# Performance work log

Measured on AMD Instinct MI355X. Metric: run time of the kernel, lower is better.

The kernel has to match this reference:

```python
import jax, jax.numpy as jnp
import numpy as np

B, C_IN, C_OUT, H, W = 32, 64, 64, 128, 128
K, KH, KW = 4, 3, 3
HID = max(8, C_IN // 4)  # reduction=4 -> 16


def setup_inputs() -> dict:
    key = jax.random.key(0)
    ks = jax.random.split(key, 16)
    s = lambda k, shape, scale=0.1: jax.random.normal(k, shape, dtype=jnp.float32) * scale
    inp = {
        "x": jax.random.normal(ks[0], (B, C_IN, H, W), dtype=jnp.float32),
        "weight": s(ks[1], (K, C_OUT, C_IN, KH, KW)),  # static weight bank
        "bias": s(ks[2], (C_OUT,)),
        "mlp_w": s(ks[3], (HID, C_IN)),
        "mlp_b": s(ks[4], (HID,)),
        "wK": s(ks[5], (K, HID)),  "bK": s(ks[6], (K,)),
        "wO": s(ks[7], (C_OUT, HID)), "bO": s(ks[8], (C_OUT,)),
        "wI": s(ks[9], (C_IN, HID)),  "bI": s(ks[10], (C_IN,)),
        "wH": s(ks[11], (KH, HID)),   "bH": s(ks[12], (KH,)),
        "wW": s(ks[13], (KW, HID)),   "bW": s(ks[14], (KW,)),
    }
    return inp


def reference(x, weight, bias, mlp_w, mlp_b, wK, bK, wO, bO, wI, bI, wH, bH, wW, bW):
    # ---- attention branch: global avg pool -> MLP -> 5 heads ----
    g = jnp.mean(x, axis=(2, 3))                         # [B, C_in]
    h = jax.nn.relu(g @ mlp_w.T + mlp_b)                 # [B, HID]
    aK = jax.nn.softmax(h @ wK.T + bK, axis=1)           # [B, K]
    aO = jax.nn.sigmoid(h @ wO.T + bO)                   # [B, O]
    aI = jax.nn.sigmoid(h @ wI.T + bI)                   # [B, I]
    aH = jax.nn.sigmoid(h @ wH.T + bH)                   # [B, kh]
    aW = jax.nn.sigmoid(h @ wW.T + bW)                   # [B, kw]
    aH = aH / (jnp.sum(aH, axis=1, keepdims=True) + 1e-6)
    aW = aW / (jnp.sum(aW, axis=1, keepdims=True) + 1e-6)
    # fused 5-way outer product + reduction over K (same math as alpha einsum)
    w_dyn = jnp.einsum('bk,bo,bi,bh,bw,koihw->boihw', aK, aO, aI, aH, aW, weight)
    # ---- per-sample conv2d (groups=B trick expressed as vmap) ----
    def conv_one(xb, wb):
        return jax.lax.conv_general_dilated(
            xb[None], wb, window_strides=(1, 1), padding=((1, 1), (1, 1)),
            dimension_numbers=('NCHW', 'OIHW', 'NCHW'))[0]
    out = jax.vmap(conv_one)(x, w_dyn) + bias[None, :, None, None]
    return out
```

## Files before the change

### kernel.cpp

```cpp
#include <hip/hip_runtime.h>
#include <hip/hip_bf16.h>
#include <math.h>

#define BB 32
#define CI 64
#define CO 64
#define HH 128
#define WW 128
#define KK 4
#define HID 16

typedef __attribute__((ext_vector_type(8)))  __bf16 bf16x8;
typedef __attribute__((ext_vector_type(16))) float  floatx16;

__device__ __forceinline__ unsigned short f2bf(float f) {
    union { float f; unsigned int u; } a; a.f = f;
    unsigned int u = a.u;
    unsigned int r = (u + 0x7fffu + ((u >> 16) & 1u)) >> 16;
    return (unsigned short)r;
}

__global__ __launch_bounds__(256) void pool_kernel(const float* __restrict__ x,
                                                   float* __restrict__ g) {
    int bc = blockIdx.x;
    const float4* p = reinterpret_cast<const float4*>(x + (size_t)bc * (HH * WW));
    float s = 0.f;
    for (int i = threadIdx.x; i < (HH * WW) / 4; i += 256) {
        float4 v = p[i];
        s += v.x + v.y + v.z + v.w;
    }
    for (int off = 32; off > 0; off >>= 1) s += __shfl_down(s, off, 64);
    __shared__ float red[4];
    if ((threadIdx.x & 63) == 0) red[threadIdx.x >> 6] = s;
    __syncthreads();
    if (threadIdx.x == 0) {
        float tot = red[0] + red[1] + red[2] + red[3];
        g[bc] = tot * (1.0f / (HH * WW));
    }
}

__global__ __launch_bounds__(64) void attn_kernel(
    const float* __restrict__ g,
    const float* __restrict__ mlp_w, const float* __restrict__ mlp_b,
    const float* __restrict__ wK, const float* __restrict__ bK,
    const float* __restrict__ wO, const float* __restrict__ bO,
    const float* __restrict__ wI, const float* __restrict__ bI,
    const float* __restrict__ wH, const float* __restrict__ bH,
    const float* __restrict__ wW, const float* __restrict__ bW,
    float* __restrict__ aK, float* __restrict__ aO, float* __restrict__ aI,
    float* __restrict__ aH, float* __restrict__ aW) {
    int b = blockIdx.x;
    int t = threadIdx.x;
    __shared__ float sg[CI];
    __shared__ float sh[HID];
    __shared__ float sK[KK];
    __shared__ float sH[3];
    __shared__ float sW[3];

    sg[t] = g[b * CI + t];
    __syncthreads();

    if (t < HID) {
        float s = mlp_b[t];
        for (int c = 0; c < CI; c++) s = fmaf(mlp_w[t * CI + c], sg[c], s);
        sh[t] = fmaxf(s, 0.f);
    }
    __syncthreads();

    {
        float sO = bO[t], sI = bI[t];
        for (int j = 0; j < HID; j++) {
            float hv = sh[j];
            sO = fmaf(wO[t * HID + j], hv, sO);
            sI = fmaf(wI[t * HID + j], hv, sI);
        }
        aO[b * CO + t] = 1.f / (1.f + expf(-sO));
        aI[b * CI + t] = 1.f / (1.f + expf(-sI));
    }
    if (t < KK) {
        float s = bK[t];
        for (int j = 0; j < HID; j++) s = fmaf(wK[t * HID + j], sh[j], s);
        sK[t] = s;
    }
    if (t < 3) {
        float s = bH[t];
        for (int j = 0; j < HID; j++) s = fmaf(wH[t * HID + j], sh[j], s);
        sH[t] = 1.f / (1.f + expf(-s));
        float s2 = bW[t];
        for (int j = 0; j < HID; j++) s2 = fmaf(wW[t * HID + j], sh[j], s2);
        sW[t] = 1.f / (1.f + expf(-s2));
    }
    __syncthreads();

    if (t == 0) {
        float m = fmaxf(fmaxf(sK[0], sK[1]), fmaxf(sK[2], sK[3]));
        float e0 = expf(sK[0] - m), e1 = expf(sK[1] - m);
        float e2 = expf(sK[2] - m), e3 = expf(sK[3] - m);
        float s = e0 + e1 + e2 + e3;
        aK[b * KK + 0] = e0 / s;
        aK[b * KK + 1] = e1 / s;
        aK[b * KK + 2] = e2 / s;
        aK[b * KK + 3] = e3 / s;
        float hs = sH[0] + sH[1] + sH[2] + 1e-6f;
        float wsum = sW[0] + sW[1] + sW[2] + 1e-6f;
        for (int i = 0; i < 3; i++) {
            aH[b * 3 + i] = sH[i] / hs;
            aW[b * 3 + i] = sW[i] / wsum;
        }
    }
}

#define WD_TOT (BB * 9 * CO * CI)
__global__ __launch_bounds__(256) void wdyn_kernel(
    const float* __restrict__ weight,
    const float* __restrict__ aK, const float* __restrict__ aO,
    const float* __restrict__ aI, const float* __restrict__ aH,
    const float* __restrict__ aW, unsigned short* __restrict__ wdbf) {
    int idx = blockIdx.x * 256 + threadIdx.x;
    if (idx >= WD_TOT) return;
    int i   = idx & 63;
    int o   = (idx >> 6) & 63;
    int bt  = idx >> 12;
    int tap = bt % 9;
    int b   = bt / 9;

    int wbase = (o * CI + i) * 9 + tap;
    const float* ak = aK + b * KK;
    float s = 0.f;
#pragma unroll
    for (int k = 0; k < KK; k++) s = fmaf(ak[k], weight[k * (CO * CI * 9) + wbase], s);
    float v = s * aO[b * CO + o] * aI[b * CI + i] *
              aH[b * 3 + tap / 3] * aW[b * 3 + tap % 3];
    wdbf[idx] = f2bf(v);
}

#define ICCH 16
#define PADI 24
#define SX_ELE (6 * 130 * PADI)
#define SW_ELE (9 * 64 * PADI)

__global__ __launch_bounds__(512, 4) void conv_kernel(
    const float* __restrict__ x, const unsigned short* __restrict__ wdbf,
    const float* __restrict__ bias, float* __restrict__ out) {
    const int y0 = blockIdx.x * 4;
    const int b  = blockIdx.y;
    const int t  = threadIdx.x;
    const int lane = t & 63;
    const int w    = t >> 6;
    const int ry   = w >> 1;
    const int c0   = (w & 1) * 64;
    const int l31  = lane & 31;
    const int koct = lane >> 5;

    __shared__ __align__(16) unsigned short sx[SX_ELE];
    __shared__ __align__(16) unsigned short sw[SW_ELE];

    floatx16 acc[2][2];
#pragma unroll
    for (int i = 0; i < 2; i++)
#pragma unroll
        for (int j = 0; j < 2; j++)
#pragma unroll
            for (int q = 0; q < 16; q++) acc[i][j][q] = 0.f;

    const float* xb = x + (size_t)b * CI * HH * WW;
    const unsigned short* wdb = wdbf + (size_t)b * 9 * CO * CI;

    const int pA0 = (0 * 32 + l31) * PADI + koct * 8;
    const int pA1 = (1 * 32 + l31) * PADI + koct * 8;
    const int pB0 = (ry * 130 + c0 + 0  + l31) * PADI + koct * 8;
    const int pB1 = (ry * 130 + c0 + 32 + l31) * PADI + koct * 8;

    for (int chunk = 0; chunk < 4; chunk++) {
        const int ic0 = chunk * ICCH;
        __syncthreads();
        for (int idx = t; idx < 6 * 130 * 8; idx += 512) {
            int c  = idx % 130;
            int t2 = idx / 130;
            int r  = t2 % 6;
            int icp = t2 / 6;
            int gy = y0 - 1 + r;
            int gx = c - 1;
            float f0 = 0.f, f1 = 0.f;
            if ((unsigned)gy < (unsigned)HH && (unsigned)gx < (unsigned)WW) {
                const float* xp = xb + (size_t)(ic0 + icp * 2) * (HH * WW) + gy * WW + gx;
                f0 = xp[0];
                f1 = xp[HH * WW];
            }
            unsigned int pk = (unsigned int)f2bf(f0) | ((unsigned int)f2bf(f1) << 16);
            *reinterpret_cast<unsigned int*>(&sx[(r * 130 + c) * PADI + icp * 2]) = pk;
        }
        for (int idx = t; idx < 9 * 64 * 2; idx += 512) {
            int k8  = idx & 1;
            int oc  = (idx >> 1) & 63;
            int tap = idx >> 7;
            const uint4 v = *reinterpret_cast<const uint4*>(
                wdb + ((tap * 64 + oc) * 64 + ic0 + k8 * 8));
            *reinterpret_cast<uint4*>(&sw[(tap * 64 + oc) * PADI + k8 * 8]) = v;
        }
        __syncthreads();

#pragma unroll
        for (int kh = 0; kh < 3; kh++) {
#pragma unroll
            for (int kw = 0; kw < 3; kw++) {
                const int tap  = kh * 3 + kw;
                const int aoff = tap * (64 * PADI);
                const int boff = (kh * 130 + kw) * PADI;
                bf16x8 a0 = *reinterpret_cast<const bf16x8*>(&sw[pA0 + aoff]);
                bf16x8 a1 = *reinterpret_cast<const bf16x8*>(&sw[pA1 + aoff]);
                bf16x8 b0 = *reinterpret_cast<const bf16x8*>(&sx[pB0 + boff]);
                bf16x8 b1 = *reinterpret_cast<const bf16x8*>(&sx[pB1 + boff]);
                acc[0][0] = __builtin_amdgcn_mfma_f32_32x32x16_bf16(a0, b0, acc[0][0], 0, 0, 0);
                acc[0][1] = __builtin_amdgcn_mfma_f32_32x32x16_bf16(a0, b1, acc[0][1], 0, 0, 0);
                acc[1][0] = __builtin_amdgcn_mfma_f32_32x32x16_bf16(a1, b0, acc[1][0], 0, 0, 0);
                acc[1][1] = __builtin_amdgcn_mfma_f32_32x32x16_bf16(a1, b1, acc[1][1], 0, 0, 0);
            }
        }
    }

    const int y = y0 + ry;
    float* ob = out + (size_t)b * CO * HH * WW + (size_t)y * WW;
#pragma unroll
    for (int mt = 0; mt < 2; mt++) {
#pragma unroll
        for (int r = 0; r < 16; r++) {
            int oc = mt * 32 + (r & 3) + 8 * (r >> 2) + 4 * koct;
            float bv = bias[oc];
            ob[(size_t)oc * (HH * WW) + c0 + l31]      = acc[mt][0][r] + bv;
            ob[(size_t)oc * (HH * WW) + c0 + l31 + 32] = acc[mt][1][r] + bv;
        }
    }
}

extern "C" void kernel_launch(void* const* d_in, const int* in_sizes, int n_in,
                              void* d_out, int out_size, void* d_ws, size_t ws_size,
                              hipStream_t stream) {
    const float* x     = (const float*)d_in[0];
    const float* weight= (const float*)d_in[1];
    const float* bias  = (const float*)d_in[2];
    const float* mlp_w = (const float*)d_in[3];
    const float* mlp_b = (const float*)d_in[4];
    const float* wK    = (const float*)d_in[5];
    const float* bK    = (const float*)d_in[6];
    const float* wO    = (const float*)d_in[7];
    const float* bO    = (const float*)d_in[8];
    const float* wI    = (const float*)d_in[9];
    const float* bI    = (const float*)d_in[10];
    const float* wH    = (const float*)d_in[11];
    const float* bH    = (const float*)d_in[12];
    const float* wW    = (const float*)d_in[13];
    const float* bW    = (const float*)d_in[14];
    float* out = (float*)d_out;

    float* ws = (float*)d_ws;
    float* g  = ws;
    float* aK = g + 2048;
    float* aO = aK + 128;
    float* aI = aO + 2048;
    float* aH = aI + 2048;
    float* aW = aH + 96;
    unsigned short* wdbf = (unsigned short*)(ws + 8192);

    pool_kernel<<<BB * CI, 256, 0, stream>>>(x, g);
    attn_kernel<<<BB, 64, 0, stream>>>(g, mlp_w, mlp_b, wK, bK, wO, bO, wI, bI,
                                       wH, bH, wW, bW, aK, aO, aI, aH, aW);
    wdyn_kernel<<<(WD_TOT + 255) / 256, 256, 0, stream>>>(weight, aK, aO, aI, aH, aW, wdbf);
    conv_kernel<<<dim3(HH / 4, BB), 512, 0, stream>>>(x, wdbf, bias, out);
}
```

Measured before the change: 335.4 us.

## Pre-convert input to padded channel-last bf16 and read conv operands from global

A new prepass kernel converts x into a padded NHWC-style bf16 buffer, split into 16-channel groups, and accumulates the global average pool with atomics. This replaces the separate pool kernel. The conv kernel now loads B fragments directly from global/L2 instead of staging fp32 input tiles through LDS with per-element conversion, and each block covers 8 rows with 4 column tiles per wave. wdyn is restructured to stage the weight bank in shared memory and write in the new grouped layout. The cost is an extra full-tensor bf16 write and re-read, float atomics in the pooling, and lower occupancy from the larger accumulator count.

Result: slower. 363.3 us (+8.3%).

```diff
diff --git a/kernel.cpp b/kernel.cpp
--- a/kernel.cpp
+++ b/kernel.cpp
@@ -20,22 +20,48 @@
     return (unsigned short)r;
 }
 
-__global__ __launch_bounds__(256) void pool_kernel(const float* __restrict__ x,
-                                                   float* __restrict__ g) {
-    int bc = blockIdx.x;
-    const float4* p = reinterpret_cast<const float4*>(x + (size_t)bc * (HH * WW));
-    float s = 0.f;
-    for (int i = threadIdx.x; i < (HH * WW) / 4; i += 256) {
-        float4 v = p[i];
-        s += v.x + v.y + v.z + v.w;
-    }
-    for (int off = 32; off > 0; off >>= 1) s += __shfl_down(s, off, 64);
-    __shared__ float red[4];
-    if ((threadIdx.x & 63) == 0) red[threadIdx.x >> 6] = s;
-    __syncthreads();
-    if (threadIdx.x == 0) {
-        float tot = red[0] + red[1] + red[2] + red[3];
-        g[bc] = tot * (1.0f / (HH * WW));
+#define XROW 130
+#define XPLANE (128 * XROW * 16)
+
+__global__ __launch_bounds__(256) void prepass_kernel(
+    const float* __restrict__ x, unsigned short* __restrict__ xbf,
+    float* __restrict__ g) {
+    const int y = blockIdx.x;
+    const int b = blockIdx.y;
+    const int t = threadIdx.x;
+    __shared__ __align__(16) unsigned short tile[128 * 72];
+
+    for (int j = 0; j < 8; j++) {
+        int idx = t + j * 256;
+        int ic = idx >> 5;
+        int xq = idx & 31;
+        const float4 v = *reinterpret_cast<const float4*>(
+            x + (((size_t)(b * CI + ic)) * HH + y) * WW + xq * 4);
+        tile[(xq * 4 + 0) * 72 + ic] = f2bf(v.x);
+        tile[(xq * 4 + 1) * 72 + ic] = f2bf(v.y);
+        tile[(xq * 4 + 2) * 72 + ic] = f2bf(v.z);
+        tile[(xq * 4 + 3) * 72 + ic] = f2bf(v.w);
+        float s = v.x + v.y + v.z + v.w;
+        for (int off = 16; off > 0; off >>= 1) s += __shfl_down(s, off, 32);
+        if ((t & 31) == 0) atomicAdd(&g[b * CI + ic], s * (1.0f / (HH * WW)));
+    }
+    __syncthreads();
+
+    unsigned short* dst_b = xbf + (size_t)b * 4 * XPLANE + (size_t)y * (XROW * 16);
+    for (int j = 0; j < 4; j++) {
+        int idx = t + j * 256;
+        int h  = idx & 1;
+        int xp = (idx >> 1) & 127;
+        int gg = idx >> 8;
+        uint4 v = *reinterpret_cast<const uint4*>(&tile[xp * 72 + gg * 16 + h * 8]);
+        *reinterpret_cast<uint4*>(dst_b + (size_t)gg * XPLANE + (xp + 1) * 16 + h * 8) = v;
+    }
+    if (t < 16) {
+        int h  = t & 1;
+        int gg = (t >> 1) & 3;
+        int xi = (t >> 3) * 129;
+        uint4 z = make_uint4(0, 0, 0, 0);
+        *reinterpret_cast<uint4*>(dst_b + (size_t)gg * XPLANE + xi * 16 + h * 8) = z;
     }
 }
 
@@ -110,125 +136,124 @@
     }
 }
 
-#define WD_TOT (BB * 9 * CO * CI)
 __global__ __launch_bounds__(256) void wdyn_kernel(
     const float* __restrict__ weight,
     const float* __restrict__ aK, const float* __restrict__ aO,
     const float* __restrict__ aI, const float* __restrict__ aH,
     const float* __restrict__ aW, unsigned short* __restrict__ wdbf) {
-    int idx = blockIdx.x * 256 + threadIdx.x;
-    if (idx >= WD_TOT) return;
-    int i   = idx & 63;
-    int o   = (idx >> 6) & 63;
-    int bt  = idx >> 12;
-    int tap = bt % 9;
-    int b   = bt / 9;
-
-    int wbase = (o * CI + i) * 9 + tap;
-    const float* ak = aK + b * KK;
-    float s = 0.f;
-#pragma unroll
-    for (int k = 0; k < KK; k++) s = fmaf(ak[k], weight[k * (CO * CI * 9) + wbase], s);
-    float v = s * aO[b * CO + o] * aI[b * CI + i] *
-              aH[b * 3 + tap / 3] * aW[b * 3 + tap % 3];
-    wdbf[idx] = f2bf(v);
-}
-
-#define ICCH 16
-#define PADI 24
-#define SX_ELE (6 * 130 * PADI)
-#define SW_ELE (9 * 64 * PADI)
-
-__global__ __launch_bounds__(512, 4) void conv_kernel(
-    const float* __restrict__ x, const unsigned short* __restrict__ wdbf,
+    const int o  = blockIdx.x;
+    const int bg = blockIdx.y;
+    const int t  = threadIdx.x;
+    __shared__ float sw4[4 * 576];
+    __shared__ float sI[8][64];
+    __shared__ float sK4[8][4];
+    __shared__ float sO[8];
+    __shared__ float sH3[8][3];
+    __shared__ float sW3[8][3];
+
+    for (int idx = t; idx < 4 * 576; idx += 256) {
+        int k = idx / 576, r = idx % 576;
+        sw4[idx] = weight[((size_t)(k * CO + o)) * 576 + r];
+    }
+    for (int idx = t; idx < 8 * 64; idx += 256) {
+        int bl = idx >> 6, i = idx & 63;
+        sI[bl][i] = aI[(bg * 8 + bl) * CI + i];
+    }
+    if (t < 8)  sO[t] = aO[(bg * 8 + t) * CO + o];
+    if (t < 32) sK4[t >> 2][t & 3] = aK[(bg * 8 + (t >> 2)) * KK + (t & 3)];
+    if (t >= 64 && t < 88)  sH3[(t - 64) / 3][(t - 64) % 3] = aH[(bg * 8 + (t - 64) / 3) * 3 + (t - 64) % 3];
+    if (t >= 96 && t < 120) sW3[(t - 96) / 3][(t - 96) % 3] = aW[(bg * 8 + (t - 96) / 3) * 3 + (t - 96) % 3];
+    __syncthreads();
+
+    for (int bl = 0; bl < 8; bl++) {
+        const int b = bg * 8 + bl;
+        for (int idx = t; idx < 576; idx += 256) {
+            int icw = idx & 15;
+            int tq  = idx >> 4;
+            int tap = tq % 9;
+            int gg  = tq / 9;
+            int i   = gg * 16 + icw;
+            float s = sK4[bl][0] * sw4[0 * 576 + i * 9 + tap]
+                    + sK4[bl][1] * sw4[1 * 576 + i * 9 + tap]
+                    + sK4[bl][2] * sw4[2 * 576 + i * 9 + tap]
+                    + sK4[bl][3] * sw4[3 * 576 + i * 9 + tap];
+            float v = s * sO[bl] * sI[bl][i] * sH3[bl][tap / 3] * sW3[bl][tap % 3];
+            wdbf[((((size_t)b * 4 + gg) * 9 + tap) * CO + o) * 16 + icw] = f2bf(v);
+        }
+    }
+}
+
+__global__ __launch_bounds__(512, 2) void conv_kernel(
+    const unsigned short* __restrict__ xbf,
+    const unsigned short* __restrict__ wdbf,
     const float* __restrict__ bias, float* __restrict__ out) {
-    const int y0 = blockIdx.x * 4;
+    const int y0 = blockIdx.x * 8;
     const int b  = blockIdx.y;
     const int t  = threadIdx.x;
     const int lane = t & 63;
     const int w    = t >> 6;
-    const int ry   = w >> 1;
-    const int c0   = (w & 1) * 64;
     const int l31  = lane & 31;
     const int koct = lane >> 5;
 
-    __shared__ __align__(16) unsigned short sx[SX_ELE];
-    __shared__ __align__(16) unsigned short sw[SW_ELE];
-
-    floatx16 acc[2][2];
+    __shared__ __align__(16) unsigned short sw[9 * 64 * 24];
+
+    floatx16 acc[2][4];
 #pragma unroll
     for (int i = 0; i < 2; i++)
 #pragma unroll
-        for (int j = 0; j < 2; j++)
+        for (int j = 0; j < 4; j++)
 #pragma unroll
             for (int q = 0; q < 16; q++) acc[i][j][q] = 0.f;
 
-    const float* xb = x + (size_t)b * CI * HH * WW;
-    const unsigned short* wdb = wdbf + (size_t)b * 9 * CO * CI;
-
-    const int pA0 = (0 * 32 + l31) * PADI + koct * 8;
-    const int pA1 = (1 * 32 + l31) * PADI + koct * 8;
-    const int pB0 = (ry * 130 + c0 + 0  + l31) * PADI + koct * 8;
-    const int pB1 = (ry * 130 + c0 + 32 + l31) * PADI + koct * 8;
-
-    for (int chunk = 0; chunk < 4; chunk++) {
-        const int ic0 = chunk * ICCH;
+    const unsigned short* xb_b = xbf + (size_t)b * 4 * XPLANE;
+
+    for (int g = 0; g < 4; g++) {
         __syncthreads();
-        for (int idx = t; idx < 6 * 130 * 8; idx += 512) {
-            int c  = idx % 130;
-            int t2 = idx / 130;
-            int r  = t2 % 6;
-            int icp = t2 / 6;
-            int gy = y0 - 1 + r;
-            int gx = c - 1;
-            float f0 = 0.f, f1 = 0.f;
-            if ((unsigned)gy < (unsigned)HH && (unsigned)gx < (unsigned)WW) {
-                const float* xp = xb + (size_t)(ic0 + icp * 2) * (HH * WW) + gy * WW + gx;
-                f0 = xp[0];
-                f1 = xp[HH * WW];
-            }
-            unsigned int pk = (unsigned int)f2bf(f0) | ((unsigned int)f2bf(f1) << 16);
-            *reinterpret_cast<unsigned int*>(&sx[(r * 130 + c) * PADI + icp * 2]) = pk;
-        }
-        for (int idx = t; idx < 9 * 64 * 2; idx += 512) {
-            int k8  = idx & 1;
+        const unsigned short* wdp = wdbf + (((size_t)b * 4 + g) * 9 * CO * 16);
+        for (int idx = t; idx < 1152; idx += 512) {
+            int h   = idx & 1;
             int oc  = (idx >> 1) & 63;
             int tap = idx >> 7;
-            const uint4 v = *reinterpret_cast<const uint4*>(
-                wdb + ((tap * 64 + oc) * 64 + ic0 + k8 * 8));
-            *reinterpret_cast<uint4*>(&sw[(tap * 64 + oc) * PADI + k8 * 8]) = v;
+            uint4 v = *reinterpret_cast<const uint4*>(wdp + idx * 8);
+            *reinterpret_cast<uint4*>(&sw[(tap * 64 + oc) * 24 + h * 8]) = v;
         }
         __syncthreads();
 
+        const unsigned short* gplane = xb_b + (size_t)g * XPLANE;
 #pragma unroll
         for (int kh = 0; kh < 3; kh++) {
-#pragma unroll
-            for (int kw = 0; kw < 3; kw++) {
-                const int tap  = kh * 3 + kw;
-                const int aoff = tap * (64 * PADI);
-                const int boff = (kh * 130 + kw) * PADI;
-                bf16x8 a0 = *reinterpret_cast<const bf16x8*>(&sw[pA0 + aoff]);
-                bf16x8 a1 = *reinterpret_cast<const bf16x8*>(&sw[pA1 + aoff]);
-                bf16x8 b0 = *reinterpret_cast<const bf16x8*>(&sx[pB0 + boff]);
-                bf16x8 b1 = *reinterpret_cast<const bf16x8*>(&sx[pB1 + boff]);
-                acc[0][0] = __builtin_amdgcn_mfma_f32_32x32x16_bf16(a0, b0, acc[0][0], 0, 0, 0);
-                acc[0][1] = __builtin_amdgcn_mfma_f32_32x32x16_bf16(a0, b1, acc[0][1], 0, 0, 0);
-                acc[1][0] = __builtin_amdgcn_mfma_f32_32x32x16_bf16(a1, b0, acc[1][0], 0, 0, 0);
-                acc[1][1] = __builtin_amdgcn_mfma_f32_32x32x16_bf16(a1, b1, acc[1][1], 0, 0, 0);
+            const int row = y0 + w + kh - 1;
+            if ((unsigned)row < (unsigned)HH) {
+                const unsigned short* rp =
+                    gplane + ((size_t)row * XROW + l31) * 16 + koct * 8;
+#pragma unroll
+                for (int kw = 0; kw < 3; kw++) {
+                    const int tap = kh * 3 + kw;
+                    bf16x8 a0 = *reinterpret_cast<const bf16x8*>(&sw[(tap * 64 + l31) * 24 + koct * 8]);
+                    bf16x8 a1 = *reinterpret_cast<const bf16x8*>(&sw[(tap * 64 + 32 + l31) * 24 + koct * 8]);
+#pragma unroll
+                    for (int pt = 0; pt < 4; pt++) {
+                        bf16x8 bf = *reinterpret_cast<const bf16x8*>(rp + (pt * 32 + kw) * 16);
+                        acc[0][pt] = __builtin_amdgcn_mfma_f32_32x32x16_bf16(a0, bf, acc[0][pt], 0, 0, 0);
+                        acc[1][pt] = __builtin_amdgcn_mfma_f32_32x32x16_bf16(a1, bf, acc[1][pt], 0, 0, 0);
+                    }
+                }
             }
         }
     }
 
-    const int y = y0 + ry;
+    const int y = y0 + w;
     float* ob = out + (size_t)b * CO * HH * WW + (size_t)y * WW;
 #pragma unroll
     for (int mt = 0; mt < 2; mt++) {
 #pragma unroll
         for (int r = 0; r < 16; r++) {
-            int oc = mt * 32 + (r & 3) + 8 * (r >> 2) + 4 * koct;
-            float bv = bias[oc];
-            ob[(size_t)oc * (HH * WW) + c0 + l31]      = acc[mt][0][r] + bv;
-            ob[(size_t)oc * (HH * WW) + c0 + l31 + 32] = acc[mt][1][r] + bv;
+            const int oc = mt * 32 + (r & 3) + 8 * (r >> 2) + 4 * koct;
+            const float bv = bias[oc];
+#pragma unroll
+            for (int pt = 0; pt < 4; pt++) {
+                ob[(size_t)oc * (HH * WW) + pt * 32 + l31] = acc[mt][pt][r] + bv;
+            }
         }
     }
 }
@@ -261,10 +286,12 @@
     float* aH = aI + 2048;
     float* aW = aH + 96;
     unsigned short* wdbf = (unsigned short*)(ws + 8192);
-
-    pool_kernel<<<BB * CI, 256, 0, stream>>>(x, g);
+    unsigned short* xbf  = wdbf + (size_t)BB * 4 * 9 * CO * 16;
+
+    hipMemsetAsync(g, 0, 2048 * sizeof(float), stream);
+    prepass_kernel<<<dim3(HH, BB), 256, 0, stream>>>(x, xbf, g);
     attn_kernel<<<BB, 64, 0, stream>>>(g, mlp_w, mlp_b, wK, bK, wO, bO, wI, bI,
                                        wH, bH, wW, bW, aK, aO, aI, aH, aW);
-    wdyn_kernel<<<(WD_TOT + 255) / 256, 256, 0, stream>>>(weight, aK, aO, aI, aH, aW, wdbf);
-    conv_kernel<<<dim3(HH / 4, BB), 512, 0, stream>>>(x, wdbf, bias, out);
-}
+    wdyn_kernel<<<dim3(CO, 4), 256, 0, stream>>>(weight, aK, aO, aI, aH, aW, wdbf);
+    conv_kernel<<<dim3(HH / 8, BB), 512, 0, stream>>>(xbf, wdbf, bias, out);
+}
```
